# Optimization experiments

Hardware: AMD Instinct MI355X
Metric: run time of the kernel (lower is better)

Reference implementation:

```python
import jax, jax.numpy as jnp
import numpy as np
from jax import lax

# program token ids
PAD, START, END, SCENE, INTERSECT, FILT, RELATE, QUERY = range(8)
SKIP = (PAD, START, END)


def conv2d(x, w, b, dil=1):
    # 'same' padding for odd kernels (3x3 pad=dil, 1x1 pad=0), NCHW/OIHW
    pad = dil * (w.shape[2] // 2)
    y = lax.conv_general_dilated(x, w, (1, 1), [(pad, pad), (pad, pad)],
                                 rhs_dilation=(dil, dil),
                                 dimension_numbers=('NCHW', 'OIHW', 'NCHW'))
    return y + b[None, :, None, None]


def maxpool2(x):
    return lax.reduce_window(x, -jnp.inf, lax.max, (1, 1, 2, 2), (1, 1, 2, 2), 'VALID')


def exec_program(prog, feat_input, p):
    """Run one (concrete) program over a batch of stem features. prog: tuple of ints,
    executed in reversed order exactly like TbDNet.forward."""
    B, _, H, W = feat_input.shape
    output = feat_input
    saved = None
    for t in reversed(prog):
        if t in SKIP:
            continue
        if t == SCENE:
            saved = output
            output = jnp.ones((B, 1, H, W), feat_input.dtype)
        elif t == INTERSECT:  # AndModule: elementwise min of attentions
            output = jnp.minimum(output, saved)
        elif t == FILT:
            a = feat_input * output  # [B,D,H,W] * [B,1,H,W]
            a = jax.nn.relu(conv2d(a, p['att_w1'], p['att_b1']))
            a = jax.nn.relu(conv2d(a, p['att_w2'], p['att_b2']))
            output = jax.nn.sigmoid(conv2d(a, p['att_w3'], p['att_b3']))
        elif t == RELATE:  # RelateModule: dilated conv stack (1,2,4,8,1) -> conv1x1 sigmoid
            a = feat_input * output
            for w, b, d in ((p['rel_w1'], p['rel_b1'], 1), (p['rel_w2'], p['rel_b2'], 2),
                            (p['rel_w3'], p['rel_b3'], 4), (p['rel_w4'], p['rel_b4'], 8),
                            (p['rel_w5'], p['rel_b5'], 1)):
                a = jax.nn.relu(conv2d(a, w, b, d))
            output = jax.nn.sigmoid(conv2d(a, p['rel_w6'], p['rel_b6']))
        elif t == QUERY:
            a = feat_input * output
            a = jax.nn.relu(conv2d(a, p['qry_w1'], p['qry_b1']))
            output = jax.nn.relu(conv2d(a, p['qry_w2'], p['qry_b2']))
    return output


def tbd_forward(feats, programs_np, p):
    B = feats.shape[0]
    stem = jax.nn.relu(conv2d(feats, p['stem_w1'], p['stem_b1']))
    stem = jax.nn.relu(conv2d(stem, p['stem_w2'], p['stem_b2']))  # [B,D,H,W]
    D, H, W = stem.shape[1], stem.shape[2], stem.shape[3]
    # group samples by identical program so dispatch runs batched, not per-sample
    groups = {}
    for n in range(B):
        groups.setdefault(tuple(int(v) for v in programs_np[n]), []).append(n)
    mod_out = jnp.zeros((B, D, H, W), feats.dtype)
    for prog, idxs in groups.items():
        idx = jnp.array(idxs)
        mod_out = mod_out.at[idx].set(exec_program(prog, stem[idx], p))
    # classifier: conv1x1 -> relu -> maxpool2 -> flatten -> fc -> relu -> fc
    x = jax.nn.relu(conv2d(mod_out, p['cls_w'], p['cls_b']))
    x = maxpool2(x)                        # [B,1024,7,7]
    x = x.reshape(B, -1)                   # [B,50176]
    x = jax.nn.relu(x @ p['fc1_w'].T + p['fc1_b'])
    return x @ p['fc2_w'].T + p['fc2_b']   # [B,28]


def setup_inputs() -> dict:
    key = jax.random.key(0)
    ks = iter(jax.random.split(key, 64))
    def rn(shape, s=0.05):
        return jax.random.normal(next(ks), shape, dtype=jnp.float32) * s
    B, Cin, H, W, D, P, L, A = 64, 1024, 14, 14, 128, 1024, 1024, 28
    feats = jax.random.normal(next(ks), (B, Cin, H, W), dtype=jnp.float32)
    # stored programs; execution order is reversed(stored)
    progA = [START, QUERY, FILT, RELATE, FILT, SCENE, END, PAD]            # scene->filter->relate->filter->query
    progB = [START, QUERY, INTERSECT, FILT, SCENE, FILT, SCENE, END]       # two filter branches -> intersect -> query
    programs = jnp.array([progA] * (B // 2) + [progB] * (B // 2), dtype=jnp.int32)
    inp = {'feats': feats, 'programs': programs,
           'stem_w1': rn((D, Cin, 3, 3), 0.02), 'stem_b1': rn((D,)),
           'stem_w2': rn((D, D, 3, 3)), 'stem_b2': rn((D,)),
           'att_w1': rn((D, D, 3, 3)), 'att_b1': rn((D,)),
           'att_w2': rn((D, D, 3, 3)), 'att_b2': rn((D,)),
           'att_w3': rn((1, D, 1, 1)), 'att_b3': rn((1,)),
           'rel_w1': rn((D, D, 3, 3)), 'rel_b1': rn((D,)),
           'rel_w2': rn((D, D, 3, 3)), 'rel_b2': rn((D,)),
           'rel_w3': rn((D, D, 3, 3)), 'rel_b3': rn((D,)),
           'rel_w4': rn((D, D, 3, 3)), 'rel_b4': rn((D,)),
           'rel_w5': rn((D, D, 3, 3)), 'rel_b5': rn((D,)),
           'rel_w6': rn((1, D, 1, 1)), 'rel_b6': rn((1,)),
           'qry_w1': rn((D, D, 3, 3)), 'qry_b1': rn((D,)),
           'qry_w2': rn((D, D, 3, 3)), 'qry_b2': rn((D,)),
           'cls_w': rn((P, D, 1, 1)), 'cls_b': rn((P,)),
           'fc1_w': rn((L, P * (H // 2) * (W // 2)), 0.01), 'fc1_b': rn((L,)),
           'fc2_w': rn((A, L)), 'fc2_b': rn((A,))}
    return inp


PARAM_NAMES = ['stem_w1', 'stem_b1', 'stem_w2', 'stem_b2',
               'att_w1', 'att_b1', 'att_w2', 'att_b2', 'att_w3', 'att_b3',
               'rel_w1', 'rel_b1', 'rel_w2', 'rel_b2', 'rel_w3', 'rel_b3',
               'rel_w4', 'rel_b4', 'rel_w5', 'rel_b5', 'rel_w6', 'rel_b6',
               'qry_w1', 'qry_b1', 'qry_w2', 'qry_b2',
               'cls_w', 'cls_b', 'fc1_w', 'fc1_b', 'fc2_w', 'fc2_b']


def reference(feats, programs, stem_w1, stem_b1, stem_w2, stem_b2,
              att_w1, att_b1, att_w2, att_b2, att_w3, att_b3,
              rel_w1, rel_b1, rel_w2, rel_b2, rel_w3, rel_b3,
              rel_w4, rel_b4, rel_w5, rel_b5, rel_w6, rel_b6,
              qry_w1, qry_b1, qry_w2, qry_b2,
              cls_w, cls_b, fc1_w, fc1_b, fc2_w, fc2_b):
    vals = [stem_w1, stem_b1, stem_w2, stem_b2,
            att_w1, att_b1, att_w2, att_b2, att_w3, att_b3,
            rel_w1, rel_b1, rel_w2, rel_b2, rel_w3, rel_b3,
            rel_w4, rel_b4, rel_w5, rel_b5, rel_w6, rel_b6,
            qry_w1, qry_b1, qry_w2, qry_b2,
            cls_w, cls_b, fc1_w, fc1_b, fc2_w, fc2_b]
    p = dict(zip(PARAM_NAMES, vals))
    return tbd_forward(feats, np.asarray(programs), p)
```

## Files before the change

### kernel.cpp

```cpp
#include <hip/hip_runtime.h>
#include <math.h>


typedef __attribute__((ext_vector_type(8)))  short   short8;
typedef __attribute__((ext_vector_type(8)))  __bf16  bf16x8;
typedef __attribute__((ext_vector_type(4)))  float   f32x4;

#define NROUNDS 15
#define NKS 49

#define B_WSTEM1 0UL
#define B_WSTEM2 2359296UL
#define B_WMOD   2654208UL
#define B_WCLS   5308416UL
#define B_STEM   5570560UL
#define B_XA     8781824UL
#define B_XB     11993088UL
#define B_FEAT   15204352UL
#define B_ATTN   18415616UL
#define B_SAVED  18465792UL
#define B_SCHED  18515968UL
#define B_ACTB   18520064UL
#define B_FC1T   24942592UL
#define B_S1P    B_XB
#define B_FC1P   B_STEM

__device__ __forceinline__ unsigned short f2bf(float f) {
    unsigned int b = __float_as_uint(f);
    b += 0x7fffu + ((b >> 16) & 1u);
    return (unsigned short)(b >> 16);
}
__device__ __forceinline__ float bf2f(unsigned short u) {
    return __uint_as_float(((unsigned int)u) << 16);
}
__device__ __forceinline__ f32x4 mfma16(bf16x8 a, bf16x8 b, f32x4 c) {
    return __builtin_amdgcn_mfma_f32_16x16x32_bf16(a, b, c, 0, 0, 0);
}

struct RepackArgs { const float* src[12]; };

__global__ __launch_bounds__(256) void k_repack(RepackArgs a, char* ws)
{
    const int y = blockIdx.y;
    const float* __restrict__ src = a.src[y];
    int gid = blockIdx.x * 256 + threadIdx.x;
    int gsz = gridDim.x * 256;
    if (y == 11) {
        unsigned short* dst = (unsigned short*)(ws + B_WCLS);
        for (int i = gid; i < 131072; i += gsz) dst[i] = f2bf(src[i]);
    } else {
        const int IC = (y == 0) ? 1024 : 128;
        const int lg = (y == 0) ? 10 : 7;
        unsigned short* dst = (unsigned short*)(ws + ((y == 0) ? B_WSTEM1
                                    : (y == 1) ? B_WSTEM2
                                    : B_WMOD + (size_t)(y - 2) * 294912));
        const int total = 9 << (lg + 7);
        for (int i = gid; i < total; i += gsz) {
            int ic = i & (IC - 1);
            int oc = (i >> lg) & 127;
            int t  = i >> (lg + 7);
            dst[i] = f2bf(src[((size_t)oc * IC + ic) * 9 + t]);
        }
    }
}

__global__ __launch_bounds__(256) void k_decode_init(const int* __restrict__ prog, char* ws)
{
    int gid = blockIdx.x * 256 + threadIdx.x;
    int gsz = gridDim.x * 256;
    float* attn  = (float*)(ws + B_ATTN);
    float* saved = (float*)(ws + B_SAVED);
    for (int i = gid; i < 64 * 196; i += gsz) { attn[i] = 1.0f; saved[i] = 1.0f; }
    unsigned int* fz = (unsigned int*)(ws + B_FEAT);
    for (int i = gid; i < 64 * 25088 / 2; i += gsz) fz[i] = 0u;
    if (gid < 64) {
        int n = gid;
        int ent[NROUNDS];
        for (int r = 0; r < NROUNDS; ++r) ent[r] = 0;
        int rc = 0;
#define ENC(op,wv,dl,g,s,d) ((op)|((wv)<<4)|((dl)<<8)|((g)<<12)|((s)<<13)|((d)<<15))
#define EMIT(v) do { if (rc < NROUNDS) ent[rc++] = (v); } while (0)
        for (int j = 7; j >= 0; --j) {
            int t = prog[n * 8 + j];
            switch (t) {
                case 3: EMIT(ENC(1,0,0,0,0,0)); break;
                case 4: EMIT(ENC(2,0,0,0,0,0)); break;
                case 5:
                    EMIT(ENC(3,0,1,1,3,0));
                    EMIT(ENC(3,1,1,0,0,1));
                    EMIT(ENC(4,0,0,0,1,0));
                    break;
                case 6:
                    EMIT(ENC(3,2,1,1,3,0));
                    EMIT(ENC(3,3,2,0,0,1));
                    EMIT(ENC(3,4,4,0,1,0));
                    EMIT(ENC(3,5,8,0,0,1));
                    EMIT(ENC(3,6,1,0,1,0));
                    EMIT(ENC(4,1,0,0,0,0));
                    break;
                case 7:
                    EMIT(ENC(3,7,1,1,3,0));
                    EMIT(ENC(3,8,1,0,0,2));
                    break;
                default: break;
            }
        }
#undef EMIT
#undef ENC
        int* sched = (int*)(ws + B_SCHED);
        for (int r = 0; r < NROUNDS; ++r) sched[n * NROUNDS + r] = ent[r];
    }
}

__global__ __launch_bounds__(256) void k_stem1p(const float* __restrict__ feats,
                                                const unsigned short* __restrict__ wrep,
                                                char* ws)
{
    __shared__ unsigned short s_img[197 * 136];
    const int bx = blockIdx.x;
    const int n = bx >> 4, ks = (bx >> 2) & 3, och = (bx >> 1) & 1, pxh = bx & 1;
    const int tid = threadIdx.x, lane = tid & 63;
    const int w = tid >> 6, wm = w & 1, wn = w >> 1;
    const int l15 = lane & 15, lq = lane >> 4;

    if (tid < 68) ((unsigned int*)s_img)[196 * 68 + tid] = 0u;

    int pglob[4], pbyt[4], swz[4];
#pragma unroll
    for (int j = 0; j < 4; ++j) {
        int nt = wn + 2 * j;
        int p  = (pxh * 7 + nt) * 16 + l15;
        pglob[j] = p;
        pbyt[j] = p * 272;
        swz[j] = p & 15;
    }
    const int nNT = (wn == 0) ? 4 : 3;

    f32x4 acc[2][4];
#pragma unroll
    for (int m = 0; m < 2; ++m)
#pragma unroll
        for (int j = 0; j < 4; ++j) acc[m][j] = (f32x4){0.f, 0.f, 0.f, 0.f};

    for (int slab = 0; slab < 2; ++slab) {
        if (slab) __syncthreads();
        const float* sf = feats + ((size_t)n * 1024 + ks * 256 + slab * 128) * 196;
        for (int i = tid; i < 128 * 49; i += 256) {
            int ic = i / 49, q = i - ic * 49;
            float4 v = *(const float4*)(sf + ic * 196 + q * 4);
            int c = ic >> 3, e2 = (ic & 7) * 2;
#pragma unroll
            for (int e = 0; e < 4; ++e) {
                int p = q * 4 + e;
                int byte = p * 272 + ((c ^ (p & 15)) << 4) + e2;
                s_img[byte >> 1] = f2bf(((const float*)&v)[e]);
            }
        }
        __syncthreads();

        const int icb = ks * 256 + slab * 128;
#pragma unroll
        for (int t = 0; t < 9; ++t) {
            const int dy = t / 3 - 1, dx = t % 3 - 1;
            int baddr[4], bswz[4];
#pragma unroll
            for (int j = 0; j < 4; ++j) {
                int p = pglob[j];
                int py = (p < 196) ? (p / 14) : 1000;
                int px = p - py * 14;
                int yy = py + dy, xx = px + dx;
                bool ok = ((unsigned)yy < 14u) && ((unsigned)xx < 14u);
                int pp = p + dy * 14 + dx;
                baddr[j] = ok ? pp * 272 : 196 * 272;
                bswz[j]  = ok ? (pp & 15) : 0;
            }
#pragma unroll
            for (int kc = 0; kc < 4; ++kc) {
                const unsigned short* wt = wrep +
                    ((size_t)(t * 128 + och * 64 + wm * 32 + l15) * 1024 + icb + kc * 32 + lq * 8);
                bf16x8 a0 = *(const bf16x8*)(wt);
                bf16x8 a1 = *(const bf16x8*)(wt + 16 * 1024);
                const int cc = kc * 4 + lq;
#pragma unroll
                for (int j = 0; j < 4; ++j) {
                    if (j < nNT) {
                        bf16x8 b = *(const bf16x8*)((const char*)s_img +
                                     baddr[j] + ((cc ^ bswz[j]) << 4));
                        acc[0][j] = mfma16(a0, b, acc[0][j]);
                        acc[1][j] = mfma16(a1, b, acc[1][j]);
                    }
                }
            }
        }
    }

    unsigned short* part = (unsigned short*)(ws + B_S1P);
#pragma unroll
    for (int m = 0; m < 2; ++m) {
        const int oc = och * 64 + wm * 32 + m * 16 + lq * 4;
#pragma unroll
        for (int j = 0; j < 4; ++j) {
            if (j < nNT) {
                int p = pglob[j];
                if (p < 196) {
                    unsigned int lo = (unsigned int)f2bf(acc[m][j][0]) |
                                      ((unsigned int)f2bf(acc[m][j][1]) << 16);
                    unsigned int hi = (unsigned int)f2bf(acc[m][j][2]) |
                                      ((unsigned int)f2bf(acc[m][j][3]) << 16);
                    uint2 pk; pk.x = lo; pk.y = hi;
                    *(uint2*)(part + (((size_t)ks * 64 + n) * 196 + p) * 128 + oc) = pk;
                }
            }
        }
    }
}

__global__ __launch_bounds__(256) void k_stem1r(const char* __restrict__ ws_c,
                                                const float* __restrict__ bias,
                                                unsigned short* __restrict__ xa)
{
    int i = blockIdx.x * 256 + threadIdx.x;
    const unsigned short* part = (const unsigned short*)(ws_c + B_S1P);
    int oc8 = (i & 15) * 8;
    int np  = i >> 4;
    float s[8] = {};
#pragma unroll
    for (int ks = 0; ks < 4; ++ks) {
        short8 v = *(const short8*)(part + (((size_t)ks * 64) * 196 + np) * 128 + oc8);
#pragma unroll
        for (int e = 0; e < 8; ++e) s[e] += bf2f((unsigned short)v[e]);
    }
    short8 o;
#pragma unroll
    for (int e = 0; e < 8; ++e)
        o[e] = (short)f2bf(fmaxf(s[e] + bias[oc8 + e], 0.f));
    *(short8*)(xa + (size_t)np * 128 + oc8) = o;
}

__device__ void conv_mfma_core(const unsigned short* __restrict__ srcB,
                               const float*  __restrict__ gate,
                               const unsigned short* __restrict__ wrep,
                               const float*  __restrict__ bias,
                               unsigned short* __restrict__ dst,
                               int dil, int och, int pxh,
                               unsigned short* s_img)
{
    const int tid  = threadIdx.x, lane = tid & 63;
    const int w    = tid >> 6, wm = w & 1, wn = w >> 1;
    const int l15  = lane & 15, lq = lane >> 4;

    if (tid < 68) ((unsigned int*)s_img)[196 * 68 + tid] = 0u;

    int pglob[4], pbyt[4], pyv[4], pxv[4];
#pragma unroll
    for (int j = 0; j < 4; ++j) {
        int nt = wn + 2 * j;
        int p  = (pxh * 7 + nt) * 16 + l15;
        pglob[j] = p;
        int py = p / 14;
        pyv[j] = (p < 196) ? py : 10000;
        pxv[j] = p - py * 14;
        pbyt[j] = p * 272 + lq * 16;
    }
    const int zaddr = 196 * 272 + lq * 16;
    const int nNT = (wn == 0) ? 4 : 3;

    f32x4 acc[2][4];
#pragma unroll
    for (int m = 0; m < 2; ++m)
#pragma unroll
        for (int j = 0; j < 4; ++j) acc[m][j] = (f32x4){0.f, 0.f, 0.f, 0.f};

    if (gate) {
        for (int i = tid; i < 196 * 16; i += 256) {
            int p = i >> 4, c8 = (i & 15) * 8;
            short8 v = *(const short8*)(srcB + p * 128 + c8);
            float g = gate[p];
            short8 ov;
#pragma unroll
            for (int e = 0; e < 8; ++e)
                ov[e] = (short)f2bf(bf2f((unsigned short)v[e]) * g);
            *(short8*)(s_img + p * 136 + c8) = ov;
        }
    } else {
        for (int i = tid; i < 196 * 16; i += 256) {
            int p = i >> 4, c8 = (i & 15) * 8;
            *(short8*)(s_img + p * 136 + c8) = *(const short8*)(srcB + p * 128 + c8);
        }
    }
    __syncthreads();

    const unsigned short* wlane = wrep + (size_t)(och * 64 + wm * 32 + l15) * 128 + lq * 8;
#pragma unroll
    for (int t = 0; t < 9; ++t) {
        const int dy = (t / 3 - 1) * dil, dx = (t % 3 - 1) * dil;
        int baddr[4];
#pragma unroll
        for (int j = 0; j < 4; ++j) {
            int yy = pyv[j] + dy, xx = pxv[j] + dx;
            bool ok = ((unsigned)yy < 14u) && ((unsigned)xx < 14u);
            baddr[j] = ok ? (pbyt[j] + (dy * 14 + dx) * 272) : zaddr;
        }
        const unsigned short* wt = wlane + (size_t)(t * 128) * 128;
#pragma unroll
        for (int kc = 0; kc < 4; ++kc) {
            bf16x8 a0 = *(const bf16x8*)(wt + kc * 32);
            bf16x8 a1 = *(const bf16x8*)(wt + (size_t)16 * 128 + kc * 32);
#pragma unroll
            for (int j = 0; j < 4; ++j) {
                if (j < nNT) {
                    bf16x8 b = *(const bf16x8*)((const char*)s_img + baddr[j] + kc * 64);
                    acc[0][j] = mfma16(a0, b, acc[0][j]);
                    acc[1][j] = mfma16(a1, b, acc[1][j]);
                }
            }
        }
    }

#pragma unroll
    for (int m = 0; m < 2; ++m) {
        const int oc = och * 64 + wm * 32 + m * 16 + lq * 4;
        const float4 b4 = *(const float4*)(bias + oc);
#pragma unroll
        for (int j = 0; j < 4; ++j) {
            if (j < nNT) {
                int p = pglob[j];
                if (p < 196) {
                    float v0 = fmaxf(acc[m][j][0] + b4.x, 0.f);
                    float v1 = fmaxf(acc[m][j][1] + b4.y, 0.f);
                    float v2 = fmaxf(acc[m][j][2] + b4.z, 0.f);
                    float v3 = fmaxf(acc[m][j][3] + b4.w, 0.f);
                    unsigned int lo = (unsigned int)f2bf(v0) | ((unsigned int)f2bf(v1) << 16);
                    unsigned int hi = (unsigned int)f2bf(v2) | ((unsigned int)f2bf(v3) << 16);
                    uint2 pk; pk.x = lo; pk.y = hi;
                    *(uint2*)(dst + p * 128 + oc) = pk;
                }
            }
        }
    }
}

__global__ __launch_bounds__(256) void k_conv_stem2(const unsigned short* __restrict__ srcBall,
                                                    const unsigned short* __restrict__ wrep,
                                                    const float* __restrict__ bias,
                                                    unsigned short* __restrict__ dstall)
{
    __shared__ unsigned short s_img[197 * 136];
    const int n = blockIdx.x >> 2, och = (blockIdx.x >> 1) & 1, pxh = blockIdx.x & 1;
    conv_mfma_core(srcBall + (size_t)n * 25088, nullptr, wrep, bias,
                   dstall + (size_t)n * 25088, 1, och, pxh, s_img);
}

struct RArgs {
    char* ws;
    const float* mbias[9];
    const float* w1x1[2];
    const float* b1x1[2];
};

__global__ __launch_bounds__(256) void k_round(RArgs a, int r)
{
    __shared__ unsigned short s_img[197 * 136];
    const int bx = blockIdx.x;
    const int n = bx >> 2, och = (bx >> 1) & 1, pxh = bx & 1;
    char* ws = a.ws;
    const int* sched = (const int*)(ws + B_SCHED);
    const int e = sched[n * NROUNDS + r];
    const int op = e & 15;
    if (op == 0) return;
    float* attn  = (float*)(ws + B_ATTN)  + n * 196;
    float* saved = (float*)(ws + B_SAVED) + n * 196;
    if (op == 1 || op == 2) {
        if ((bx & 3) == 0 && threadIdx.x < 196) {
            int p = threadIdx.x;
            if (op == 1) { saved[p] = attn[p]; attn[p] = 1.0f; }
            else         attn[p] = fminf(attn[p], saved[p]);
        }
        return;
    }
    const int wset = (e >> 4) & 15, dil = (e >> 8) & 15, gatef = (e >> 12) & 1;
    const int srcid = (e >> 13) & 3, dstid = (e >> 15) & 3;
    const unsigned short* src = (const unsigned short*)(ws +
            (srcid == 3 ? B_STEM : srcid == 1 ? B_XB : B_XA)) + (size_t)n * 25088;
    if (op == 4) {
        if ((bx & 3) == 0 && threadIdx.x < 196) {
            int p = threadIdx.x;
            const float* wv = a.w1x1[wset];
            float acc = a.b1x1[wset][0];
            const unsigned short* row = src + p * 128;
#pragma unroll 8
            for (int ic = 0; ic < 128; ++ic) acc += bf2f(row[ic]) * wv[ic];
            attn[p] = 1.0f / (1.0f + __expf(-acc));
        }
        return;
    }
    unsigned short* dst = (unsigned short*)(ws +
            (dstid == 2 ? B_FEAT : dstid == 1 ? B_XB : B_XA)) + (size_t)n * 25088;
    const unsigned short* wrep = (const unsigned short*)(ws + B_WMOD) + (size_t)wset * 9 * 128 * 128;
    conv_mfma_core(src, gatef ? attn : nullptr, wrep, a.mbias[wset], dst,
                   dil, och, pxh, s_img);
}

__global__ __launch_bounds__(256) void k_cls_pool(const unsigned short* __restrict__ featall,
                                                  const unsigned short* __restrict__ clsw,
                                                  const float* __restrict__ clsb,
                                                  unsigned short* __restrict__ actB)
{
    __shared__ char smem[197 * 272 + 64 * 200 * 4];
    unsigned short* s_img = (unsigned short*)smem;
    float* s_pool = (float*)(smem + 197 * 272);
    const int n = blockIdx.x >> 4, pt = blockIdx.x & 15;
    const int tid = threadIdx.x, lane = tid & 63, w = tid >> 6;
    const int l15 = lane & 15, lq = lane >> 4;
    const unsigned short* feat = featall + (size_t)n * 25088;

    if (tid < 68) ((unsigned int*)s_img)[196 * 68 + tid] = 0u;
    for (int i = tid; i < 196 * 16; i += 256) {
        int p = i >> 4, c8 = (i & 15) * 8;
        *(short8*)(s_img + p * 136 + c8) = *(const short8*)(feat + p * 128 + c8);
    }
    f32x4 acc[14];
#pragma unroll
    for (int j = 0; j < 14; ++j) acc[j] = (f32x4){0.f, 0.f, 0.f, 0.f};
    __syncthreads();

    const unsigned short* wl = clsw + (size_t)(pt * 64 + w * 16 + l15) * 128 + lq * 8;
#pragma unroll
    for (int kc = 0; kc < 4; ++kc) {
        bf16x8 a0 = *(const bf16x8*)(wl + kc * 32);
#pragma unroll
        for (int j = 0; j < 14; ++j) {
            int p = j * 16 + l15;
            int ba = (p < 196) ? (p * 272 + lq * 16 + kc * 64) : (196 * 272 + lq * 16);
            bf16x8 b = *(const bf16x8*)((const char*)s_img + ba);
            acc[j] = mfma16(a0, b, acc[j]);
        }
    }
    const int oc = pt * 64 + w * 16 + lq * 4;
    const float4 b4 = *(const float4*)(clsb + oc);
    const int pl = w * 16 + lq * 4;
#pragma unroll
    for (int j = 0; j < 14; ++j) {
        int p = j * 16 + l15;
        if (p < 196) {
            s_pool[(pl + 0) * 200 + p] = fmaxf(acc[j][0] + b4.x, 0.f);
            s_pool[(pl + 1) * 200 + p] = fmaxf(acc[j][1] + b4.y, 0.f);
            s_pool[(pl + 2) * 200 + p] = fmaxf(acc[j][2] + b4.z, 0.f);
            s_pool[(pl + 3) * 200 + p] = fmaxf(acc[j][3] + b4.w, 0.f);
        }
    }
    __syncthreads();
    for (int i = tid; i < 64 * 49; i += 256) {
        int plx = i / 49, q = i - plx * 49;
        int py = q / 7, qx = q - py * 7;
        const float* rp = s_pool + plx * 200 + py * 28 + qx * 2;
        float m = fmaxf(fmaxf(rp[0], rp[1]), fmaxf(rp[14], rp[15]));
        int k = (pt * 64 + plx) * 49 + q;
        int kb = k >> 6, lq2 = (k >> 4) & 3, hi = (k >> 3) & 1, e = k & 7;
        actB[((((size_t)kb * 4 + lq2) * 2 + hi) * 64 + n) * 8 + e] = f2bf(m);
    }
}

__global__ __launch_bounds__(256) void k_fc1p(const unsigned short* __restrict__ actB,
                                              const float* __restrict__ w,
                                              float* __restrict__ part)
{
    const int jt = blockIdx.x & 15, ks = blockIdx.x >> 4;
    const int tid = threadIdx.x, lane = tid & 63, wv = tid >> 6;
    const int l15 = lane & 15, lq = lane >> 4;
    const int k0 = ks * 1024;
    const int j = jt * 64 + wv * 16 + l15;

    f32x4 acc[4];
#pragma unroll
    for (int t = 0; t < 4; ++t) acc[t] = (f32x4){0.f, 0.f, 0.f, 0.f};

    const float* wrow = w + (size_t)j * 50176 + k0 + lq * 16;
    const int kb0 = k0 >> 6;

#pragma unroll 4
    for (int kc = 0; kc < 1024; kc += 64) {
        const float* wp = wrow + kc;
        float4 f0 = *(const float4*)(wp);
        float4 f1 = *(const float4*)(wp + 4);
        float4 f2 = *(const float4*)(wp + 8);
        float4 f3 = *(const float4*)(wp + 12);
        bf16x8 a0, a1;
        a0[0] = (__bf16)f0.x; a0[1] = (__bf16)f0.y; a0[2] = (__bf16)f0.z; a0[3] = (__bf16)f0.w;
        a0[4] = (__bf16)f1.x; a0[5] = (__bf16)f1.y; a0[6] = (__bf16)f1.z; a0[7] = (__bf16)f1.w;
        a1[0] = (__bf16)f2.x; a1[1] = (__bf16)f2.y; a1[2] = (__bf16)f2.z; a1[3] = (__bf16)f2.w;
        a1[4] = (__bf16)f3.x; a1[5] = (__bf16)f3.y; a1[6] = (__bf16)f3.z; a1[7] = (__bf16)f3.w;
        const int kb = kb0 + (kc >> 6);
        const unsigned short* bp0 = actB + (((size_t)kb * 4 + lq) * 2) * 512 + l15 * 8;
#pragma unroll
        for (int t = 0; t < 4; ++t) {
            bf16x8 b0 = *(const bf16x8*)(bp0 + t * 128);
            bf16x8 b1 = *(const bf16x8*)(bp0 + 512 + t * 128);
            acc[t] = mfma16(a0, b0, acc[t]);
            acc[t] = mfma16(a1, b1, acc[t]);
        }
    }

    float* pbase = part + ((size_t)ks * 1024 + jt * 64 + wv * 16 + lq * 4) * 64 + l15;
#pragma unroll
    for (int t = 0; t < 4; ++t)
#pragma unroll
        for (int r = 0; r < 4; ++r)
            pbase[(size_t)r * 64 + t * 16] = acc[t][r];
}

__global__ __launch_bounds__(256) void k_fc1r(const float* __restrict__ part,
                                              const float* __restrict__ b,
                                              float* __restrict__ fc1T)
{
    int i = blockIdx.x * 256 + threadIdx.x;
    if (i >= 65536) return;
    float s = 0.0f;
    for (int ks = 0; ks < NKS; ++ks) s += part[(size_t)ks * 65536 + i];
    int j = i >> 6;
    fc1T[i] = fmaxf(s + b[j], 0.0f);
}

__global__ __launch_bounds__(256) void k_fc2(const float* __restrict__ fc1T,
                                             const float* __restrict__ w,
                                             const float* __restrict__ b,
                                             float* __restrict__ out)
{
    __shared__ float red[256];
    const int a_ = blockIdx.x;
    const int tid = threadIdx.x, lane = tid & 63, q = tid >> 6;
    float acc = 0.0f;
    const float* wr = w + (size_t)a_ * 1024;
    for (int k = q * 256; k < q * 256 + 256; ++k)
        acc = fmaf(fc1T[k * 64 + lane], wr[k], acc);
    red[tid] = acc;
    __syncthreads();
    if (q == 0) {
        float s = red[tid] + red[tid + 64] + red[tid + 128] + red[tid + 192] + b[a_];
        out[lane * 28 + a_] = s;
    }
}

extern "C" void kernel_launch(void* const* d_in, const int* in_sizes, int n_in,
                              void* d_out, int out_size, void* d_ws, size_t ws_size,
                              hipStream_t stream)
{
    const float* feats = (const float*)d_in[0];
    const int*   prog  = (const int*)d_in[1];
    char* ws  = (char*)d_ws;
    float* out = (float*)d_out;

    RepackArgs ra;
    ra.src[0]  = (const float*)d_in[2];
    ra.src[1]  = (const float*)d_in[4];
    ra.src[2]  = (const float*)d_in[6];
    ra.src[3]  = (const float*)d_in[8];
    ra.src[4]  = (const float*)d_in[12];
    ra.src[5]  = (const float*)d_in[14];
    ra.src[6]  = (const float*)d_in[16];
    ra.src[7]  = (const float*)d_in[18];
    ra.src[8]  = (const float*)d_in[20];
    ra.src[9]  = (const float*)d_in[24];
    ra.src[10] = (const float*)d_in[26];
    ra.src[11] = (const float*)d_in[28];

    k_repack<<<dim3(64, 12), 256, 0, stream>>>(ra, ws);

    k_stem1p<<<1024, 256, 0, stream>>>(feats, (const unsigned short*)(ws + B_WSTEM1), ws);
    k_stem1r<<<784, 256, 0, stream>>>(ws, (const float*)d_in[3],
                                      (unsigned short*)(ws + B_XA));

    k_decode_init<<<256, 256, 0, stream>>>(prog, ws);

    k_conv_stem2<<<256, 256, 0, stream>>>((const unsigned short*)(ws + B_XA),
                                          (const unsigned short*)(ws + B_WSTEM2),
                                          (const float*)d_in[5],
                                          (unsigned short*)(ws + B_STEM));

    RArgs ga;
    ga.ws = ws;
    ga.mbias[0] = (const float*)d_in[7];
    ga.mbias[1] = (const float*)d_in[9];
    ga.mbias[2] = (const float*)d_in[13];
    ga.mbias[3] = (const float*)d_in[15];
    ga.mbias[4] = (const float*)d_in[17];
    ga.mbias[5] = (const float*)d_in[19];
    ga.mbias[6] = (const float*)d_in[21];
    ga.mbias[7] = (const float*)d_in[25];
    ga.mbias[8] = (const float*)d_in[27];
    ga.w1x1[0]  = (const float*)d_in[10];
    ga.w1x1[1]  = (const float*)d_in[22];
    ga.b1x1[0]  = (const float*)d_in[11];
    ga.b1x1[1]  = (const float*)d_in[23];

    for (int r = 0; r < NROUNDS; ++r)
        k_round<<<256, 256, 0, stream>>>(ga, r);

    k_cls_pool<<<1024, 256, 0, stream>>>((const unsigned short*)(ws + B_FEAT),
                                         (const unsigned short*)(ws + B_WCLS),
                                         (const float*)d_in[29],
                                         (unsigned short*)(ws + B_ACTB));
    k_fc1p<<<784, 256, 0, stream>>>((const unsigned short*)(ws + B_ACTB),
                                    (const float*)d_in[30], (float*)(ws + B_FC1P));
    k_fc1r<<<256, 256, 0, stream>>>((const float*)(ws + B_FC1P), (const float*)d_in[31],
                                    (float*)(ws + B_FC1T));
    k_fc2<<<28, 256, 0, stream>>>((const float*)(ws + B_FC1T), (const float*)d_in[32],
                                  (const float*)d_in[33], out);
}
```

Baseline: 598.3 us.

## Coalesce stem1 image staging and stage fc1 weights through LDS with prefetch

In the stem conv kernel, the feature image is now staged by loading four channels per thread and writing packed 8-byte LDS stores into a padded, unswizzled layout. The per-tap address math is simplified by precomputing pixel row and column. In the fc1 partial GEMM, each block now loads the fp32 weight tile with row-contiguous coalesced float4 reads into a register prefetch buffer. It converts the tile to bf16 in shared memory and double-buffers the next chunk through registers, so the strided per-lane weight reads of the old loop go away. The costs are extra syncthreads, higher register pressure from the prefetch array, and possible LDS bank conflicts from dropping the swizzle.

```diff
diff --git a/kernel.cpp b/kernel.cpp
--- a/kernel.cpp
+++ b/kernel.cpp
@@ -125,15 +125,18 @@
 
     if (tid < 68) ((unsigned int*)s_img)[196 * 68 + tid] = 0u;
 
-    int pglob[4], pbyt[4], swz[4];
+    int pglob[4], pbyt[4], pyv[4], pxv[4];
 #pragma unroll
     for (int j = 0; j < 4; ++j) {
         int nt = wn + 2 * j;
         int p  = (pxh * 7 + nt) * 16 + l15;
         pglob[j] = p;
-        pbyt[j] = p * 272;
-        swz[j] = p & 15;
-    }
+        int py = p / 14;
+        pyv[j] = (p < 196) ? py : 10000;
+        pxv[j] = p - py * 14;
+        pbyt[j] = p * 272 + lq * 16;
+    }
+    const int zaddr = 196 * 272 + lq * 16;
     const int nNT = (wn == 0) ? 4 : 3;
 
     f32x4 acc[2][4];
@@ -141,38 +144,40 @@
     for (int m = 0; m < 2; ++m)
 #pragma unroll
         for (int j = 0; j < 4; ++j) acc[m][j] = (f32x4){0.f, 0.f, 0.f, 0.f};
+
+    const int icg = tid & 31;
 
     for (int slab = 0; slab < 2; ++slab) {
         if (slab) __syncthreads();
-        const float* sf = feats + ((size_t)n * 1024 + ks * 256 + slab * 128) * 196;
-        for (int i = tid; i < 128 * 49; i += 256) {
-            int ic = i / 49, q = i - ic * 49;
-            float4 v = *(const float4*)(sf + ic * 196 + q * 4);
-            int c = ic >> 3, e2 = (ic & 7) * 2;
+        const int icb = ks * 256 + slab * 128;
+        const float* sf = feats + ((size_t)n * 1024 + icb) * 196;
+        for (int qq = (tid >> 5); qq < 49; qq += 8) {
+            const float* p0 = sf + icg * 4 * 196 + qq * 4;
+            float4 r0 = *(const float4*)(p0);
+            float4 r1 = *(const float4*)(p0 + 196);
+            float4 r2 = *(const float4*)(p0 + 392);
+            float4 r3 = *(const float4*)(p0 + 588);
 #pragma unroll
             for (int e = 0; e < 4; ++e) {
-                int p = q * 4 + e;
-                int byte = p * 272 + ((c ^ (p & 15)) << 4) + e2;
-                s_img[byte >> 1] = f2bf(((const float*)&v)[e]);
+                uint2 v;
+                v.x = (unsigned int)f2bf(((const float*)&r0)[e]) |
+                      ((unsigned int)f2bf(((const float*)&r1)[e]) << 16);
+                v.y = (unsigned int)f2bf(((const float*)&r2)[e]) |
+                      ((unsigned int)f2bf(((const float*)&r3)[e]) << 16);
+                *(uint2*)(s_img + (qq * 4 + e) * 136 + icg * 4) = v;
             }
         }
         __syncthreads();
 
-        const int icb = ks * 256 + slab * 128;
 #pragma unroll
         for (int t = 0; t < 9; ++t) {
             const int dy = t / 3 - 1, dx = t % 3 - 1;
-            int baddr[4], bswz[4];
+            int baddr[4];
 #pragma unroll
             for (int j = 0; j < 4; ++j) {
-                int p = pglob[j];
-                int py = (p < 196) ? (p / 14) : 1000;
-                int px = p - py * 14;
-                int yy = py + dy, xx = px + dx;
+                int yy = pyv[j] + dy, xx = pxv[j] + dx;
                 bool ok = ((unsigned)yy < 14u) && ((unsigned)xx < 14u);
-                int pp = p + dy * 14 + dx;
-                baddr[j] = ok ? pp * 272 : 196 * 272;
-                bswz[j]  = ok ? (pp & 15) : 0;
+                baddr[j] = ok ? (pbyt[j] + (dy * 14 + dx) * 272) : zaddr;
             }
 #pragma unroll
             for (int kc = 0; kc < 4; ++kc) {
@@ -180,12 +185,10 @@
                     ((size_t)(t * 128 + och * 64 + wm * 32 + l15) * 1024 + icb + kc * 32 + lq * 8);
                 bf16x8 a0 = *(const bf16x8*)(wt);
                 bf16x8 a1 = *(const bf16x8*)(wt + 16 * 1024);
-                const int cc = kc * 4 + lq;
 #pragma unroll
                 for (int j = 0; j < 4; ++j) {
                     if (j < nNT) {
-                        bf16x8 b = *(const bf16x8*)((const char*)s_img +
-                                     baddr[j] + ((cc ^ bswz[j]) << 4));
+                        bf16x8 b = *(const bf16x8*)((const char*)s_img + baddr[j] + kc * 64);
                         acc[0][j] = mfma16(a0, b, acc[0][j]);
                         acc[1][j] = mfma16(a1, b, acc[1][j]);
                     }
@@ -465,41 +468,69 @@
                                               const float* __restrict__ w,
                                               float* __restrict__ part)
 {
+    __shared__ unsigned short s_w[64 * 264];
     const int jt = blockIdx.x & 15, ks = blockIdx.x >> 4;
     const int tid = threadIdx.x, lane = tid & 63, wv = tid >> 6;
     const int l15 = lane & 15, lq = lane >> 4;
     const int k0 = ks * 1024;
-    const int j = jt * 64 + wv * 16 + l15;
+    const int r4 = tid & 3, l4 = (tid >> 2) & 15, rw = tid >> 6;
 
     f32x4 acc[4];
 #pragma unroll
     for (int t = 0; t < 4; ++t) acc[t] = (f32x4){0.f, 0.f, 0.f, 0.f};
 
-    const float* wrow = w + (size_t)j * 50176 + k0 + lq * 16;
-    const int kb0 = k0 >> 6;
-
-#pragma unroll 4
-    for (int kc = 0; kc < 1024; kc += 64) {
-        const float* wp = wrow + kc;
-        float4 f0 = *(const float4*)(wp);
-        float4 f1 = *(const float4*)(wp + 4);
-        float4 f2 = *(const float4*)(wp + 8);
-        float4 f3 = *(const float4*)(wp + 12);
-        bf16x8 a0, a1;
-        a0[0] = (__bf16)f0.x; a0[1] = (__bf16)f0.y; a0[2] = (__bf16)f0.z; a0[3] = (__bf16)f0.w;
-        a0[4] = (__bf16)f1.x; a0[5] = (__bf16)f1.y; a0[6] = (__bf16)f1.z; a0[7] = (__bf16)f1.w;
-        a1[0] = (__bf16)f2.x; a1[1] = (__bf16)f2.y; a1[2] = (__bf16)f2.z; a1[3] = (__bf16)f2.w;
-        a1[4] = (__bf16)f3.x; a1[5] = (__bf16)f3.y; a1[6] = (__bf16)f3.z; a1[7] = (__bf16)f3.w;
-        const int kb = kb0 + (kc >> 6);
-        const unsigned short* bp0 = actB + (((size_t)kb * 4 + lq) * 2) * 512 + l15 * 8;
-#pragma unroll
-        for (int t = 0; t < 4; ++t) {
-            bf16x8 b0 = *(const bf16x8*)(bp0 + t * 128);
-            bf16x8 b1 = *(const bf16x8*)(bp0 + 512 + t * 128);
-            acc[t] = mfma16(a0, b0, acc[t]);
-            acc[t] = mfma16(a1, b1, acc[t]);
-        }
-    }
+    float4 pf[4][4];
+
+#define FC1_LOAD(ss_) do {                                                        \
+    _Pragma("unroll")                                                             \
+    for (int pass = 0; pass < 4; ++pass) {                                        \
+        const int row_ = pass * 16 + rw * 4 + r4;                                 \
+        const float* wp_ = w + (size_t)(jt * 64 + row_) * 50176 + k0              \
+                             + (ss_) * 256 + l4 * 16;                             \
+        pf[pass][0] = *(const float4*)(wp_);                                      \
+        pf[pass][1] = *(const float4*)(wp_ + 4);                                  \
+        pf[pass][2] = *(const float4*)(wp_ + 8);                                  \
+        pf[pass][3] = *(const float4*)(wp_ + 12);                                 \
+    } } while (0)
+
+    FC1_LOAD(0);
+
+    for (int ss = 0; ss < 4; ++ss) {
+        __syncthreads();
+#pragma unroll
+        for (int pass = 0; pass < 4; ++pass) {
+            const int row = pass * 16 + rw * 4 + r4;
+            bf16x8 c0, c1;
+            c0[0] = (__bf16)pf[pass][0].x; c0[1] = (__bf16)pf[pass][0].y;
+            c0[2] = (__bf16)pf[pass][0].z; c0[3] = (__bf16)pf[pass][0].w;
+            c0[4] = (__bf16)pf[pass][1].x; c0[5] = (__bf16)pf[pass][1].y;
+            c0[6] = (__bf16)pf[pass][1].z; c0[7] = (__bf16)pf[pass][1].w;
+            c1[0] = (__bf16)pf[pass][2].x; c1[1] = (__bf16)pf[pass][2].y;
+            c1[2] = (__bf16)pf[pass][2].z; c1[3] = (__bf16)pf[pass][2].w;
+            c1[4] = (__bf16)pf[pass][3].x; c1[5] = (__bf16)pf[pass][3].y;
+            c1[6] = (__bf16)pf[pass][3].z; c1[7] = (__bf16)pf[pass][3].w;
+            *(bf16x8*)(s_w + row * 264 + l4 * 16)     = c0;
+            *(bf16x8*)(s_w + row * 264 + l4 * 16 + 8) = c1;
+        }
+        __syncthreads();
+        if (ss < 3) FC1_LOAD(ss + 1);
+
+        const unsigned short* arow = s_w + (wv * 16 + l15) * 264;
+#pragma unroll
+        for (int kk = 0; kk < 8; ++kk) {
+            bf16x8 a = *(const bf16x8*)(arow + kk * 32 + lq * 8);
+            const int kglob = k0 + ss * 256 + kk * 32 + lq * 8;
+            const int kb = kglob >> 6, lq2 = (kglob >> 4) & 3, hi = (kglob >> 3) & 1;
+            const unsigned short* bp = actB +
+                ((((size_t)kb * 4 + lq2) * 2 + hi) * 64 + l15) * 8;
+#pragma unroll
+            for (int t = 0; t < 4; ++t) {
+                bf16x8 b = *(const bf16x8*)(bp + t * 128);
+                acc[t] = mfma16(a, b, acc[t]);
+            }
+        }
+    }
+#undef FC1_LOAD
 
     float* pbase = part + ((size_t)ks * 1024 + jt * 64 + wv * 16 + lq * 4) * 64 + l15;
 #pragma unroll
```

New measurement: 598.9 us. No clear change (+0.1%).
